# Kernel optimization log

Hardware: AMD Instinct MI355X
Metric: run time of the kernel (lower is better)

The kernel has to match this reference:

```python
import jax, jax.numpy as jnp
import numpy as np

N = 50000   # nodes
E = 800000  # edges (avg degree 16)
IN = 256    # in_dim
H = 1       # num_heads
D = 96      # hid_dim
OUT = 128   # out_dim (LSTM hidden)


def setup_inputs() -> dict:
    key = jax.random.key(0)
    ks = jax.random.split(key, 14)
    s = 0.05
    return {
        "x": jax.random.normal(ks[0], (N, IN), jnp.float32),
        "W_fc": jax.random.normal(ks[1], (IN, H * D), jnp.float32) * s,
        "attn_l": jax.random.normal(ks[2], (H, D), jnp.float32) * s,
        "attn_r": jax.random.normal(ks[3], (H, D), jnp.float32) * s,
        "bias": jax.random.normal(ks[4], (H * D,), jnp.float32) * s,
        "W_ih": jax.random.normal(ks[5], (4 * OUT, D), jnp.float32) * s,
        "W_hh": jax.random.normal(ks[6], (4 * OUT, OUT), jnp.float32) * s,
        "b_ih": jax.random.normal(ks[7], (4 * OUT,), jnp.float32) * s,
        "b_hh": jax.random.normal(ks[8], (4 * OUT,), jnp.float32) * s,
        "h0": jax.random.normal(ks[9], (1, N, OUT), jnp.float32),
        "c0": jax.random.normal(ks[10], (1, N, OUT), jnp.float32),
        "src": jax.random.randint(ks[11], (E,), 0, N, jnp.int32),
        "dst": jax.random.randint(ks[12], (E,), 0, N, jnp.int32),
    }


def reference(x, W_fc, attn_l, attn_r, bias, W_ih, W_hh, b_ih, b_hh, h0, c0, src, dst):
    # ---- GATConv breadth step ----
    feat = (x @ W_fc).reshape(N, H, D)                       # [N,H,D]
    el = jnp.einsum("nhd,hd->nh", feat, attn_l)              # [N,H]
    er = jnp.einsum("nhd,hd->nh", feat, attn_r)              # [N,H]
    e = jax.nn.leaky_relu(el[src] + er[dst], 0.2)            # [E,H]
    # edge softmax over incoming edges of each dst node
    emax = jax.ops.segment_max(e, dst, num_segments=N)       # [N,H] (-inf if empty)
    ex = jnp.exp(e - emax[dst])                              # [E,H]
    esum = jax.ops.segment_sum(ex, dst, num_segments=N)      # [N,H]
    alpha = ex / esum[dst]                                   # [E,H]
    msg = alpha[:, :, None] * feat[src]                      # [E,H,D]
    rst = jax.ops.segment_sum(msg, dst, num_segments=N)      # [N,H,D]
    rst = rst + bias.reshape(H, D)
    # ---- tanh + mean over heads ----
    xmid = jnp.tanh(rst).mean(axis=1)                        # [N,D]
    # ---- single-step LSTM (PyTorch gate order i,f,g,o) ----
    gates = xmid @ W_ih.T + b_ih + h0[0] @ W_hh.T + b_hh     # [N,4*OUT]
    i, f, g, o = jnp.split(gates, 4, axis=-1)
    c1 = jax.nn.sigmoid(f) * c0[0] + jax.nn.sigmoid(i) * jnp.tanh(g)
    h1 = jax.nn.sigmoid(o) * jnp.tanh(c1)                    # [N,OUT]
    return h1, h1[None], c1[None]
```

## Files before the change

### kernel.cpp

```cpp
#include <hip/hip_runtime.h>
#include <math.h>

#define N_NODES 50000
#define E_EDGES 800000
#define IN_DIM  256
#define D_DIM   96
#define OUT_DIM 128
#define BKT     64
#define PREP_BLOCKS 448
#define FEAT_BLOCKS 782
#define BUCK_BLOCKS 3125
#define CAST_BLOCKS 3125
#define NTILES      3125

typedef __attribute__((ext_vector_type(8))) short short8;
typedef __attribute__((ext_vector_type(4))) float f32x4;

__device__ __forceinline__ unsigned short f2bf(float f) {
    unsigned u = __float_as_uint(f);
    unsigned r = u + 0x7fffu + ((u >> 16) & 1u);
    return (unsigned short)(r >> 16);
}
__device__ __forceinline__ float bf2f(unsigned short u) {
    return __uint_as_float(((unsigned)u) << 16);
}
__device__ __forceinline__ float sigm(float x) { return 1.f / (1.f + __expf(-x)); }
__device__ __forceinline__ float ftanh(float x) { return 1.f - 2.f / (1.f + __expf(2.f * x)); }

__device__ __forceinline__ int swz(int s) { return s ^ ((s >> 4) & 7); }

__device__ __forceinline__ short8 pack8(const float* __restrict__ p) {
    float4 v0 = *(const float4*)p;
    float4 v1 = *(const float4*)(p + 4);
    union { short8 s; unsigned u[4]; } r;
    r.u[0] = (unsigned)f2bf(v0.x) | ((unsigned)f2bf(v0.y) << 16);
    r.u[1] = (unsigned)f2bf(v0.z) | ((unsigned)f2bf(v0.w) << 16);
    r.u[2] = (unsigned)f2bf(v1.x) | ((unsigned)f2bf(v1.y) << 16);
    r.u[3] = (unsigned)f2bf(v1.z) | ((unsigned)f2bf(v1.w) << 16);
    return r.s;
}

__global__ __launch_bounds__(256)
void k_prep(const float* __restrict__ Wfc, const float* __restrict__ W_ih,
            const float* __restrict__ W_hh, const float* __restrict__ b_ih,
            const float* __restrict__ b_hh,
            unsigned short* __restrict__ Wfc_frag,
            unsigned short* __restrict__ Wb_frag, float* __restrict__ bsum) {
    int tid = blockIdx.x * 256 + threadIdx.x;
    if (tid < 512) bsum[tid] = b_ih[tid] + b_hh[tid];
    if (tid < 6 * 8 * 64 * 8) {
        int j = tid & 7;
        int rest = tid >> 3;
        int l = rest & 63;
        int rest2 = rest >> 6;
        int ks = rest2 & 7;
        int cf = rest2 >> 3;
        int k   = ks * 32 + (l >> 4) * 8 + j;
        int col = cf * 16 + (l & 15);
        Wfc_frag[tid] = f2bf(Wfc[k * D_DIM + col]);
    }
    if (tid < 32 * 7 * 64 * 8) {
        int j = tid & 7;
        int rest = tid >> 3;
        int l = rest & 63;
        int rest2 = rest >> 6;
        int ks = rest2 % 7;
        int cf = rest2 / 7;
        int k   = ks * 32 + (l >> 4) * 8 + j;
        int col = cf * 16 + (l & 15);
        float v = (k < 96) ? W_ih[col * 96 + k] : W_hh[col * 128 + (k - 96)];
        Wb_frag[tid] = f2bf(v);
    }
}

__global__ __launch_bounds__(256, 2)
void k_featmm_bucket_cast(const float* __restrict__ x,
                          const unsigned short* __restrict__ Wfc_frag,
                          const float* __restrict__ al, const float* __restrict__ ar,
                          unsigned short* __restrict__ feat,
                          float* __restrict__ el, float* __restrict__ er,
                          const int* __restrict__ src, const int* __restrict__ dst,
                          int* __restrict__ cnt, unsigned short* __restrict__ ebuf16,
                          const float* __restrict__ h0, unsigned short* __restrict__ h0b) {
    if (blockIdx.x >= FEAT_BLOCKS) {
        int seg = blockIdx.x - FEAT_BLOCKS;
        if (seg < BUCK_BLOCKS) {
            int e = seg * 256 + threadIdx.x;
            if (e < E_EDGES) {
                int d = dst[e];
                int pos = atomicAdd(&cnt[d], 1);
                ebuf16[(size_t)d * BKT + pos] = (unsigned short)src[e];
            }
        } else {
            int tid = (seg - BUCK_BLOCKS) * 256 + threadIdx.x;
            if (tid < N_NODES * OUT_DIM / 8)
                *(short8*)(h0b + (size_t)tid * 8) = pack8(h0 + (size_t)tid * 8);
        }
        return;
    }
    const int t     = threadIdx.x;
    const int lane  = t & 63;
    const int w     = t >> 6;
    const int nfrag = lane & 15;
    const int khalf = lane >> 4;
    const int node  = blockIdx.x * 64 + w * 16 + nfrag;
    const int r     = min(node, N_NODES - 1);

    f32x4 acc[6];
#pragma unroll
    for (int cf = 0; cf < 6; ++cf) acc[cf] = (f32x4){0.f, 0.f, 0.f, 0.f};

    const float* px = x + (size_t)r * IN_DIM + khalf * 8;
    const unsigned short* pW = Wfc_frag + (size_t)lane * 8;

#pragma unroll 1
    for (int ks = 0; ks < 8; ++ks) {
        short8 xf = pack8(px + ks * 32);
#pragma unroll
        for (int cf = 0; cf < 6; ++cf) {
            short8 wf = *(const short8*)(pW + (size_t)((cf * 8 + ks) * 64) * 8);
            acc[cf] = __builtin_amdgcn_mfma_f32_16x16x32_bf16(wf, xf, acc[cf], 0, 0, 0);
        }
    }

    float sl = 0.f, sr = 0.f;
#pragma unroll
    for (int cf = 0; cf < 6; ++cf) {
        const int oc = cf * 16 + khalf * 4;
        const float4 a = *(const float4*)(al + oc);
        const float4 b = *(const float4*)(ar + oc);
        sl += acc[cf][0]*a.x + acc[cf][1]*a.y + acc[cf][2]*a.z + acc[cf][3]*a.w;
        sr += acc[cf][0]*b.x + acc[cf][1]*b.y + acc[cf][2]*b.z + acc[cf][3]*b.w;
    }
    sl += __shfl_xor(sl, 16, 64); sl += __shfl_xor(sl, 32, 64);
    sr += __shfl_xor(sr, 16, 64); sr += __shfl_xor(sr, 32, 64);

    if (node < N_NODES) {
        if (lane < 16) { el[node] = sl; er[node] = sr; }
#pragma unroll
        for (int cf = 0; cf < 6; ++cf) {
            const int oc = cf * 16 + khalf * 4;
            union { unsigned u[2]; } pk;
            pk.u[0] = (unsigned)f2bf(acc[cf][0]) | ((unsigned)f2bf(acc[cf][1]) << 16);
            pk.u[1] = (unsigned)f2bf(acc[cf][2]) | ((unsigned)f2bf(acc[cf][3]) << 16);
            *(uint2*)(feat + (size_t)node * D_DIM + oc) = make_uint2(pk.u[0], pk.u[1]);
        }
    }
}

__global__ __launch_bounds__(256)
void k_gather(const int* __restrict__ cnt, const unsigned short* __restrict__ ebuf16,
              const float* __restrict__ el, const float* __restrict__ er,
              const unsigned short* __restrict__ feat, const float* __restrict__ bias,
              unsigned short* __restrict__ xmid) {
    const int n    = (blockIdx.x * 256 + threadIdx.x) >> 5;
    const int lane = threadIdx.x & 31;
    if (n >= N_NODES) return;
    const size_t o0 = (size_t)n * BKT;
    const int deg = cnt[n];
    const float ern = er[n];

    float a0 = 0.f, a1 = 0.f, a2 = 0.f;
    float inv;

    if (deg <= 32) {
        int   s_l = 0;
        float v_l = -INFINITY;
        if (lane < deg) {
            s_l = ebuf16[o0 + lane];
            float v = el[s_l] + ern; v_l = v > 0.f ? v : 0.2f * v;
        }
        float vmax = v_l;
#pragma unroll
        for (int d = 16; d; d >>= 1) vmax = fmaxf(vmax, __shfl_xor(vmax, d, 32));
        float w_l = (lane < deg) ? __expf(v_l - vmax) : 0.f;
        float ssum = w_l;
#pragma unroll
        for (int d = 16; d; d >>= 1) ssum += __shfl_xor(ssum, d, 32);
        inv = 1.f / (ssum > 0.f ? ssum : 1.f);

        for (int i = 0; i < deg; ++i) {
            int   s = __shfl(s_l, i, 32);
            float w = __shfl(w_l, i, 32);
            const unsigned short* fr = feat + (size_t)s * D_DIM;
            a0 += w * bf2f(fr[lane]);
            a1 += w * bf2f(fr[lane + 32]);
            a2 += w * bf2f(fr[lane + 64]);
        }
    } else {
        float vmax = -INFINITY;
        for (int i = lane; i < deg; i += 32) {
            int s = ebuf16[o0 + i];
            float v = el[s] + ern; v = v > 0.f ? v : 0.2f * v;
            vmax = fmaxf(vmax, v);
        }
#pragma unroll
        for (int d = 16; d; d >>= 1) vmax = fmaxf(vmax, __shfl_xor(vmax, d, 32));

        float ssum = 0.f;
        for (int i = lane; i < deg; i += 32) {
            int s = ebuf16[o0 + i];
            float v = el[s] + ern; v = v > 0.f ? v : 0.2f * v;
            ssum += __expf(v - vmax);
        }
#pragma unroll
        for (int d = 16; d; d >>= 1) ssum += __shfl_xor(ssum, d, 32);
        inv = 1.f / (ssum > 0.f ? ssum : 1.f);

        for (int bi0 = 0; bi0 < deg; bi0 += 32) {
            int   i_l = bi0 + lane;
            int   s_l = 0; float w_l = 0.f;
            if (i_l < deg) {
                s_l = ebuf16[o0 + i_l];
                float v = el[s_l] + ern; v = v > 0.f ? v : 0.2f * v;
                w_l = __expf(v - vmax);
            }
            int m = min(32, deg - bi0);
            for (int i = 0; i < m; ++i) {
                int   s = __shfl(s_l, i, 32);
                float w = __shfl(w_l, i, 32);
                const unsigned short* fr = feat + (size_t)s * D_DIM;
                a0 += w * bf2f(fr[lane]);
                a1 += w * bf2f(fr[lane + 32]);
                a2 += w * bf2f(fr[lane + 64]);
            }
        }
    }

    unsigned short* zr = xmid + (size_t)n * D_DIM;
    zr[lane]      = f2bf(ftanh(a0 * inv + bias[lane]));
    zr[lane + 32] = f2bf(ftanh(a1 * inv + bias[lane + 32]));
    zr[lane + 64] = f2bf(ftanh(a2 * inv + bias[lane + 64]));
}

__global__ __launch_bounds__(256, 1)
void k_lstm_persist(const unsigned short* __restrict__ xmid,
                    const unsigned short* __restrict__ h0b,
                    const unsigned short* __restrict__ Wb_frag,
                    const float* __restrict__ bsum,
                    const float* __restrict__ cin0,
                    float* __restrict__ out_h1a, float* __restrict__ out_h1b,
                    float* __restrict__ out_c1) {
    __shared__ unsigned short wlds[16 * 7 * 64 * 8];
    __shared__ unsigned short alds[2][7 * 64 * 8];
    const int t     = threadIdx.x;
    const int lane  = t & 63;
    const int wv    = t >> 6;
    const int nfrag = lane & 15;
    const int khalf = lane >> 4;
    const int ch    = blockIdx.x >> 7;
    const int b7    = blockIdx.x & 127;

#pragma unroll 4
    for (int it = 0; it < 28; ++it) {
        int cidx = t + it * 256;
        int wg   = cidx / 448;
        int rem  = cidx % 448;
        int cf   = ch * 4 + (wg >> 2) + 8 * (wg & 3);
        *(short8*)(wlds + (size_t)cidx * 8) =
            *(const short8*)(Wb_frag + ((size_t)cf * 448 + rem) * 8);
    }

    const int oc = ch * 64 + wv * 16 + khalf * 4;
    const float4 bi = *(const float4*)(bsum + oc);
    const float4 bf = *(const float4*)(bsum + 128 + oc);
    const float4 bg = *(const float4*)(bsum + 256 + oc);
    const float4 bo = *(const float4*)(bsum + 384 + oc);

    const int U = (NTILES - b7 + 127) / 128;

    short8 r0, r1;
    int s0 = 0, s1 = 0;
    {
        int tile = b7, n0 = tile * 16;
        { int q = t;
          if (q < 192) { int rr = q / 12, ck = q % 12;
              r0 = *(const short8*)(xmid + (size_t)(n0 + rr) * D_DIM + ck * 8);
              s0 = (ck >> 2) * 64 + (ck & 3) * 16 + rr;
          } else { int p = q - 192; int rr = p >> 4, ck = p & 15;
              r0 = *(const short8*)(h0b + (size_t)(n0 + rr) * OUT_DIM + ck * 8);
              s0 = (3 + (ck >> 2)) * 64 + (ck & 3) * 16 + rr; } }
        if (t < 192) { int p = t + 64;
            int rr = p >> 4, ck = p & 15;
            r1 = *(const short8*)(h0b + (size_t)(n0 + rr) * OUT_DIM + ck * 8);
            s1 = (3 + (ck >> 2)) * 64 + (ck & 3) * 16 + rr; }
    }
    *(short8*)(alds[0] + (size_t)swz(s0) * 8) = r0;
    if (t < 192) *(short8*)(alds[0] + (size_t)swz(s1) * 8) = r1;
    __syncthreads();

    for (int u = 0; u < U; ++u) {
        const int cur  = u & 1;
        const int tile = b7 + u * 128;
        const int n0   = tile * 16;
        const int node = n0 + nfrag;

        if (u + 1 < U) {
            int nn0 = (tile + 128) * 16;
            { int q = t;
              if (q < 192) { int rr = q / 12, ck = q % 12;
                  r0 = *(const short8*)(xmid + (size_t)(nn0 + rr) * D_DIM + ck * 8);
              } else { int p = q - 192; int rr = p >> 4, ck = p & 15;
                  r0 = *(const short8*)(h0b + (size_t)(nn0 + rr) * OUT_DIM + ck * 8); } }
            if (t < 192) { int p = t + 64;
                int rr = p >> 4, ck = p & 15;
                r1 = *(const short8*)(h0b + (size_t)(nn0 + rr) * OUT_DIM + ck * 8); }
        }

        const float4 cv = *(const float4*)(cin0 + (size_t)node * OUT_DIM + oc);

        f32x4 acc[4];
#pragma unroll
        for (int g = 0; g < 4; ++g) acc[g] = (f32x4){0.f, 0.f, 0.f, 0.f};

#pragma unroll
        for (int ks = 0; ks < 7; ++ks) {
            short8 zf = *(const short8*)(alds[cur] + (size_t)swz(ks * 64 + lane) * 8);
#pragma unroll
            for (int g = 0; g < 4; ++g) {
                short8 wf = *(const short8*)(wlds +
                    (size_t)(((wv * 4 + g) * 7 + ks) * 64 + lane) * 8);
                acc[g] = __builtin_amdgcn_mfma_f32_16x16x32_bf16(wf, zf, acc[g], 0, 0, 0);
            }
        }

        {
            float4 h1, c1;
            c1.x = sigm(acc[1][0] + bf.x) * cv.x + sigm(acc[0][0] + bi.x) * ftanh(acc[2][0] + bg.x);
            c1.y = sigm(acc[1][1] + bf.y) * cv.y + sigm(acc[0][1] + bi.y) * ftanh(acc[2][1] + bg.y);
            c1.z = sigm(acc[1][2] + bf.z) * cv.z + sigm(acc[0][2] + bi.z) * ftanh(acc[2][2] + bg.z);
            c1.w = sigm(acc[1][3] + bf.w) * cv.w + sigm(acc[0][3] + bi.w) * ftanh(acc[2][3] + bg.w);
            h1.x = sigm(acc[3][0] + bo.x) * ftanh(c1.x);
            h1.y = sigm(acc[3][1] + bo.y) * ftanh(c1.y);
            h1.z = sigm(acc[3][2] + bo.z) * ftanh(c1.z);
            h1.w = sigm(acc[3][3] + bo.w) * ftanh(c1.w);
            *(float4*)(out_h1a + (size_t)node * OUT_DIM + oc) = h1;
            *(float4*)(out_h1b + (size_t)node * OUT_DIM + oc) = h1;
            *(float4*)(out_c1  + (size_t)node * OUT_DIM + oc) = c1;
        }

        if (u + 1 < U) {
            *(short8*)(alds[cur ^ 1] + (size_t)swz(s0) * 8) = r0;
            if (t < 192) *(short8*)(alds[cur ^ 1] + (size_t)swz(s1) * 8) = r1;
        }
        __syncthreads();
    }
}

extern "C" void kernel_launch(void* const* d_in, const int* in_sizes, int n_in,
                              void* d_out, int out_size, void* d_ws, size_t ws_size,
                              hipStream_t stream) {
    const float* x      = (const float*)d_in[0];
    const float* W_fc   = (const float*)d_in[1];
    const float* attn_l = (const float*)d_in[2];
    const float* attn_r = (const float*)d_in[3];
    const float* bias   = (const float*)d_in[4];
    const float* W_ih   = (const float*)d_in[5];
    const float* W_hh   = (const float*)d_in[6];
    const float* b_ih   = (const float*)d_in[7];
    const float* b_hh   = (const float*)d_in[8];
    const float* h0     = (const float*)d_in[9];
    const float* c0     = (const float*)d_in[10];
    const int*   src    = (const int*)d_in[11];
    const int*   dst    = (const int*)d_in[12];
    float* out = (float*)d_out;

    char* base = (char*)d_ws;
    unsigned short* feat     = (unsigned short*)(base);
    unsigned short* xmid     = (unsigned short*)(base + 9600000);
    unsigned short* h0b      = (unsigned short*)(base + 19200000);
    float*          el       = (float*)(base + 32000000);
    float*          er       = (float*)(base + 32200000);
    int*            cnt      = (int*)(base + 32400000);
    unsigned short* ebuf16   = (unsigned short*)(base + 32600000);
    unsigned short* Wb_frag  = (unsigned short*)(base + 39000000);
    float*          bsum     = (float*)(base + 39229376);
    unsigned short* Wfc_frag = (unsigned short*)(base + 39231424);

    hipMemsetAsync(cnt, 0, (size_t)N_NODES * sizeof(int), stream);

    k_prep<<<PREP_BLOCKS, 256, 0, stream>>>(W_fc, W_ih, W_hh, b_ih, b_hh,
                                            Wfc_frag, Wb_frag, bsum);

    k_featmm_bucket_cast<<<FEAT_BLOCKS + BUCK_BLOCKS + CAST_BLOCKS, 256, 0, stream>>>(
        x, Wfc_frag, attn_l, attn_r, feat, el, er, src, dst, cnt, ebuf16, h0, h0b);

    k_gather<<<(N_NODES * 32 + 255) / 256, 256, 0, stream>>>(cnt, ebuf16, el, er,
                                                             feat, bias, xmid);

    k_lstm_persist<<<256, 256, 0, stream>>>(xmid, h0b, Wb_frag, bsum, c0,
                                            out, out + N_NODES * OUT_DIM,
                                            out + 2 * N_NODES * OUT_DIM);
}
```

Before: 156.6 us.

## Run two independent tile groups per LSTM persistent block sharing LDS weights

The persistent LSTM kernel now launches 512 threads per block, split into two 256-thread groups. Each group processes its own interleaved stream of 16-node tiles with a private double-buffered activation tile, while both share the gate weights staged once in LDS. This halves the per-block tile loop length and doubles the waves resident per CU, which should hide global-load and MFMA latency better. The cost is twice the activation LDS, a block-wide barrier that now couples both groups, and bounds checks for the tail tiles.

```diff
diff --git a/kernel.cpp b/kernel.cpp
--- a/kernel.cpp
+++ b/kernel.cpp
@@ -233,7 +233,7 @@
     zr[lane + 64] = f2bf(ftanh(a2 * inv + bias[lane + 64]));
 }
 
-__global__ __launch_bounds__(256, 1)
+__global__ __launch_bounds__(512, 1)
 void k_lstm_persist(const unsigned short* __restrict__ xmid,
                     const unsigned short* __restrict__ h0b,
                     const unsigned short* __restrict__ Wb_frag,
@@ -242,18 +242,22 @@
                     float* __restrict__ out_h1a, float* __restrict__ out_h1b,
                     float* __restrict__ out_c1) {
     __shared__ unsigned short wlds[16 * 7 * 64 * 8];
-    __shared__ unsigned short alds[2][7 * 64 * 8];
+    __shared__ unsigned short alds[2][2][7 * 64 * 8];
     const int t     = threadIdx.x;
-    const int lane  = t & 63;
-    const int wv    = t >> 6;
+    const int grp   = t >> 8;
+    const int tl    = t & 255;
+    const int lane  = tl & 63;
+    const int wv    = tl >> 6;
     const int nfrag = lane & 15;
     const int khalf = lane >> 4;
     const int ch    = blockIdx.x >> 7;
     const int b7    = blockIdx.x & 127;
-
-#pragma unroll 4
-    for (int it = 0; it < 28; ++it) {
-        int cidx = t + it * 256;
+    const int vlane = b7 * 2 + grp;
+    const int U     = (NTILES + 255) / 256;
+
+#pragma unroll 2
+    for (int it = 0; it < 14; ++it) {
+        int cidx = t + it * 512;
         int wg   = cidx / 448;
         int rem  = cidx % 448;
         int cf   = ch * 4 + (wg >> 2) + 8 * (wg & 3);
@@ -267,64 +271,67 @@
     const float4 bg = *(const float4*)(bsum + 256 + oc);
     const float4 bo = *(const float4*)(bsum + 384 + oc);
 
-    const int U = (NTILES - b7 + 127) / 128;
+    int s0, s1 = 0;
+    {
+        int q = tl;
+        if (q < 192) { int rr = q / 12, ck = q % 12;
+            s0 = (ck >> 2) * 64 + (ck & 3) * 16 + rr;
+        } else { int p = q - 192; int rr = p >> 4, ck = p & 15;
+            s0 = (3 + (ck >> 2)) * 64 + (ck & 3) * 16 + rr; }
+        if (tl < 192) { int p = tl + 64;
+            int rr = p >> 4, ck = p & 15;
+            s1 = (3 + (ck >> 2)) * 64 + (ck & 3) * 16 + rr; }
+    }
 
     short8 r0, r1;
-    int s0 = 0, s1 = 0;
     {
-        int tile = b7, n0 = tile * 16;
-        { int q = t;
-          if (q < 192) { int rr = q / 12, ck = q % 12;
-              r0 = *(const short8*)(xmid + (size_t)(n0 + rr) * D_DIM + ck * 8);
-              s0 = (ck >> 2) * 64 + (ck & 3) * 16 + rr;
-          } else { int p = q - 192; int rr = p >> 4, ck = p & 15;
-              r0 = *(const short8*)(h0b + (size_t)(n0 + rr) * OUT_DIM + ck * 8);
-              s0 = (3 + (ck >> 2)) * 64 + (ck & 3) * 16 + rr; } }
-        if (t < 192) { int p = t + 64;
-            int rr = p >> 4, ck = p & 15;
-            r1 = *(const short8*)(h0b + (size_t)(n0 + rr) * OUT_DIM + ck * 8);
-            s1 = (3 + (ck >> 2)) * 64 + (ck & 3) * 16 + rr; }
-    }
-    *(short8*)(alds[0] + (size_t)swz(s0) * 8) = r0;
-    if (t < 192) *(short8*)(alds[0] + (size_t)swz(s1) * 8) = r1;
+        int n0 = vlane * 16;
+        if (tl < 192) { int rr = tl / 12, ck = tl % 12;
+            r0 = *(const short8*)(xmid + (size_t)(n0 + rr) * D_DIM + ck * 8);
+        } else { int p = tl - 192; int rr = p >> 4, ck = p & 15;
+            r0 = *(const short8*)(h0b + (size_t)(n0 + rr) * OUT_DIM + ck * 8); }
+        if (tl < 192) { int p = tl + 64; int rr = p >> 4, ck = p & 15;
+            r1 = *(const short8*)(h0b + (size_t)(n0 + rr) * OUT_DIM + ck * 8); }
+    }
+    *(short8*)(alds[grp][0] + (size_t)swz(s0) * 8) = r0;
+    if (tl < 192) *(short8*)(alds[grp][0] + (size_t)swz(s1) * 8) = r1;
     __syncthreads();
 
     for (int u = 0; u < U; ++u) {
-        const int cur  = u & 1;
-        const int tile = b7 + u * 128;
-        const int n0   = tile * 16;
-        const int node = n0 + nfrag;
-
-        if (u + 1 < U) {
-            int nn0 = (tile + 128) * 16;
-            { int q = t;
-              if (q < 192) { int rr = q / 12, ck = q % 12;
-                  r0 = *(const short8*)(xmid + (size_t)(nn0 + rr) * D_DIM + ck * 8);
-              } else { int p = q - 192; int rr = p >> 4, ck = p & 15;
-                  r0 = *(const short8*)(h0b + (size_t)(nn0 + rr) * OUT_DIM + ck * 8); } }
-            if (t < 192) { int p = t + 64;
-                int rr = p >> 4, ck = p & 15;
+        const int cur   = u & 1;
+        const int tile  = vlane + u * 256;
+        const bool valid  = tile < NTILES;
+        const bool nvalid = (u + 1 < U) && (tile + 256 < NTILES);
+        const int node  = tile * 16 + nfrag;
+
+        if (nvalid) {
+            int nn0 = (tile + 256) * 16;
+            if (tl < 192) { int rr = tl / 12, ck = tl % 12;
+                r0 = *(const short8*)(xmid + (size_t)(nn0 + rr) * D_DIM + ck * 8);
+            } else { int p = tl - 192; int rr = p >> 4, ck = p & 15;
+                r0 = *(const short8*)(h0b + (size_t)(nn0 + rr) * OUT_DIM + ck * 8); }
+            if (tl < 192) { int p = tl + 64; int rr = p >> 4, ck = p & 15;
                 r1 = *(const short8*)(h0b + (size_t)(nn0 + rr) * OUT_DIM + ck * 8); }
         }
 
-        const float4 cv = *(const float4*)(cin0 + (size_t)node * OUT_DIM + oc);
-
-        f32x4 acc[4];
-#pragma unroll
-        for (int g = 0; g < 4; ++g) acc[g] = (f32x4){0.f, 0.f, 0.f, 0.f};
-
-#pragma unroll
-        for (int ks = 0; ks < 7; ++ks) {
-            short8 zf = *(const short8*)(alds[cur] + (size_t)swz(ks * 64 + lane) * 8);
-#pragma unroll
-            for (int g = 0; g < 4; ++g) {
-                short8 wf = *(const short8*)(wlds +
-                    (size_t)(((wv * 4 + g) * 7 + ks) * 64 + lane) * 8);
-                acc[g] = __builtin_amdgcn_mfma_f32_16x16x32_bf16(wf, zf, acc[g], 0, 0, 0);
+        if (valid) {
+            const float4 cv = *(const float4*)(cin0 + (size_t)node * OUT_DIM + oc);
+
+            f32x4 acc[4];
+#pragma unroll
+            for (int g = 0; g < 4; ++g) acc[g] = (f32x4){0.f, 0.f, 0.f, 0.f};
+
+#pragma unroll
+            for (int ks = 0; ks < 7; ++ks) {
+                short8 zf = *(const short8*)(alds[grp][cur] + (size_t)swz(ks * 64 + lane) * 8);
+#pragma unroll
+                for (int g = 0; g < 4; ++g) {
+                    short8 wf = *(const short8*)(wlds +
+                        (size_t)(((wv * 4 + g) * 7 + ks) * 64 + lane) * 8);
+                    acc[g] = __builtin_amdgcn_mfma_f32_16x16x32_bf16(wf, zf, acc[g], 0, 0, 0);
+                }
             }
-        }
-
-        {
+
             float4 h1, c1;
             c1.x = sigm(acc[1][0] + bf.x) * cv.x + sigm(acc[0][0] + bi.x) * ftanh(acc[2][0] + bg.x);
             c1.y = sigm(acc[1][1] + bf.y) * cv.y + sigm(acc[0][1] + bi.y) * ftanh(acc[2][1] + bg.y);
@@ -339,9 +346,9 @@
             *(float4*)(out_c1  + (size_t)node * OUT_DIM + oc) = c1;
         }
 
-        if (u + 1 < U) {
-            *(short8*)(alds[cur ^ 1] + (size_t)swz(s0) * 8) = r0;
-            if (t < 192) *(short8*)(alds[cur ^ 1] + (size_t)swz(s1) * 8) = r1;
+        if (nvalid) {
+            *(short8*)(alds[grp][cur ^ 1] + (size_t)swz(s0) * 8) = r0;
+            if (tl < 192) *(short8*)(alds[grp][cur ^ 1] + (size_t)swz(s1) * 8) = r1;
         }
         __syncthreads();
     }
@@ -388,7 +395,7 @@
     k_gather<<<(N_NODES * 32 + 255) / 256, 256, 0, stream>>>(cnt, ebuf16, el, er,
                                                              feat, bias, xmid);
 
-    k_lstm_persist<<<256, 256, 0, stream>>>(xmid, h0b, Wb_frag, bsum, c0,
+    k_lstm_persist<<<256, 512, 0, stream>>>(xmid, h0b, Wb_frag, bsum, c0,
                                             out, out + N_NODES * OUT_DIM,
                                             out + 2 * N_NODES * OUT_DIM);
 }
```

New measurement: 155.1 us. No clear change (-1.0%).
